# Kernel optimization log

Hardware: AMD Instinct MI355X
Metric: run time of the kernel (lower is better)

The kernel has to match this reference:

```python
import jax, jax.numpy as jnp
import numpy as np

HEADS = 4
DIM_QK = 128
SCALE = DIM_QK ** (-0.5)


def rel_to_abs(x):
    # x: [B, Nh, L, 2L-1] -> [B, Nh, L, L] via the skew trick
    B, Nh, L, _ = x.shape
    x = jnp.pad(x, ((0, 0), (0, 0), (0, 0), (0, 1)))          # [B,Nh,L,2L]
    flat = x.reshape(B, Nh, L * 2 * L)
    flat = jnp.pad(flat, ((0, 0), (0, 0), (0, L - 1)))
    final = flat.reshape(B, Nh, L + 1, 2 * L - 1)
    return final[:, :, :L, L - 1:]


def relative_logits_1d(q, rel_k):
    # q: [B, Nh, H, W, d], rel_k: [2W-1, d] -> [B, Nh, H, H, W, W] (axes b h x i y j)
    B, Nh, H, W, _ = q.shape
    rl = jnp.einsum('bnhwd,md->bnhwm', q, rel_k)              # [B,Nh,H,W,2W-1]
    rl = rl.reshape(B, Nh * H, W, 2 * W - 1)
    rl = rel_to_abs(rl)                                        # [B,Nh*H,W,W]
    rl = rl.reshape(B, Nh, H, W, W)
    rl = jnp.broadcast_to(rl[:, :, :, None, :, :], (B, Nh, H, H, W, W))
    return rl


def rel_pos_logits(q, rel_height, rel_width, H, W):
    # q: [B, h, HW, d]
    B, h, L, d = q.shape
    qg = q.reshape(B, h, H, W, d)
    # width direction: b h x i y j -> b h (x y) (i j)
    rw = relative_logits_1d(qg, rel_width)                     # [B,h,H,H,W,W]
    rw = rw.transpose(0, 1, 2, 4, 3, 5).reshape(B, h, H * W, H * W)
    # height direction: transpose x<->y, then b h x i y j -> b h (y x) (j i)
    qh = qg.transpose(0, 1, 3, 2, 4)                           # [B,h,W,H,d]
    rh = relative_logits_1d(qh, rel_height)                    # [B,h,W,W,H,H]
    rh = rh.transpose(0, 1, 4, 2, 5, 3).reshape(B, h, H * W, H * W)
    return rw + rh


def setup_inputs() -> dict:
    key = jax.random.key(0)
    ks = jax.random.split(key, 5)
    B, C, H, W = 16, 512, 32, 32
    scale = DIM_QK ** (-0.5)
    return {
        'featuremap': jax.random.normal(ks[0], (B, C, H, W), jnp.float32),
        'w_qk': jax.random.normal(ks[1], (2 * HEADS * DIM_QK, C), jnp.float32) * (C ** -0.5),
        'w_v': jax.random.normal(ks[2], (HEADS * 128, C), jnp.float32) * (C ** -0.5),
        'rel_height': jax.random.normal(ks[3], (2 * H - 1, DIM_QK), jnp.float32) * scale,
        'rel_width': jax.random.normal(ks[4], (2 * W - 1, DIM_QK), jnp.float32) * scale,
    }


def reference(featuremap, w_qk, w_v, rel_height, rel_width):
    B, C, H, W = featuremap.shape
    L = H * W
    # 1x1 conv projections (no bias) == channel matmuls
    qk = jnp.einsum('bchw,oc->bohw', featuremap, w_qk)         # [B, 2*h*dqk, H, W]
    v = jnp.einsum('bchw,oc->bohw', featuremap, w_v)           # [B, h*dv, H, W]
    q, k = jnp.split(qk, 2, axis=1)

    def to_heads(x):
        # B (h d) H W -> B h (H W) d
        d = x.shape[1] // HEADS
        return x.reshape(B, HEADS, d, L).transpose(0, 1, 3, 2)

    q, k, v = to_heads(q), to_heads(k), to_heads(v)
    q = q * SCALE
    logits = jnp.einsum('bhxd,bhyd->bhxy', q, k)
    logits = logits + rel_pos_logits(q, rel_height, rel_width, H, W)
    weights = jax.nn.softmax(logits, axis=-1)
    attn_out = jnp.einsum('bhxy,bhyd->bhxd', weights, v)       # [B,h,L,dv]
    dv = attn_out.shape[-1]
    # B h (H W) d -> B (h d) H W
    return attn_out.transpose(0, 1, 3, 2).reshape(B, HEADS * dv, H, W)
```

## Files before the change

kernel.cpp:

```cpp
#include <hip/hip_runtime.h>
#include <stdint.h>

typedef __attribute__((ext_vector_type(4))) float f32x4;
typedef __attribute__((ext_vector_type(8))) short bf16x8;

#define DEV static __device__ __forceinline__

#define GLOAD16(g, l) __builtin_amdgcn_global_load_lds( \
    (const __attribute__((address_space(1))) void*)(g), \
    (__attribute__((address_space(3))) void*)(l), 16, 0, 0)

DEV unsigned short f2bf(float f){
  union { float f; uint32_t u; } v; v.f = f;
  return (unsigned short)((v.u + 0x7fffu + ((v.u >> 16) & 1u)) >> 16);
}

DEV uint32_t cvtpk(float a, float b){
  uint32_t r; asm("v_cvt_pk_bf16_f32 %0, %1, %2" : "=v"(r) : "v"(a), "v"(b)); return r;
}

DEV f32x4 mfma_bf16(bf16x8 a, bf16x8 b, f32x4 c){
  return __builtin_amdgcn_mfma_f32_16x16x32_bf16(a, b, c, 0, 0, 0);
}

__global__ __launch_bounds__(256) void k_transpose_cvt(const float* __restrict__ fm,
                                                       unsigned short* __restrict__ xt){
  __shared__ float tile[64][65];
  int b = blockIdx.z, c0 = blockIdx.y * 64, l0 = blockIdx.x * 64;
  int t = threadIdx.x;
  int lr = t >> 4;
  int lc4 = (t & 15) * 4;
  const float* src = fm + ((size_t)b * 512 + c0) * 1024 + l0;
  #pragma unroll
  for (int i = 0; i < 4; i++){
    int r = lr + i * 16;
    f32x4 v = *(const f32x4*)&src[(size_t)r * 1024 + lc4];
    tile[r][lc4] = v[0]; tile[r][lc4 + 1] = v[1];
    tile[r][lc4 + 2] = v[2]; tile[r][lc4 + 3] = v[3];
  }
  __syncthreads();
  int j = t & 7;
  int lrow = t >> 3;
  unsigned short* dst = xt + ((size_t)b * 1024 + l0) * 512 + c0;
  #pragma unroll
  for (int i = 0; i < 2; i++){
    int l = lrow + i * 32;
    unsigned short tmp[8];
    #pragma unroll
    for (int u = 0; u < 8; u++) tmp[u] = f2bf(tile[j * 8 + u][l]);
    *(uint4*)&dst[(size_t)l * 512 + j * 8] = *(const uint4*)tmp;
  }
}

__global__ __launch_bounds__(256) void k_wcvt(const float* __restrict__ wqk,
                                              const float* __restrict__ wv,
                                              unsigned short* __restrict__ wb){
  int idx = blockIdx.x * 256 + threadIdx.x;
  int e = idx * 4;
  if (e >= 1536 * 512) return;
  const float* src = (e < 1024 * 512) ? (wqk + e) : (wv + (e - 1024 * 512));
  f32x4 v = *(const f32x4*)src;
  unsigned short* d = wb + e;
  d[0] = f2bf(v[0]); d[1] = f2bf(v[1]); d[2] = f2bf(v[2]); d[3] = f2bf(v[3]);
}

template<int MODE>
__global__ __launch_bounds__(256, 3) void k_proj(const unsigned short* __restrict__ Abase,
                                                 const unsigned short* __restrict__ Bbase,
                                                 unsigned short* __restrict__ qbuf,
                                                 unsigned short* __restrict__ kbuf,
                                                 unsigned short* __restrict__ vbuf){
  __shared__ unsigned short Al[128][64];
  __shared__ unsigned short Bl[128][64];
  int b = blockIdx.z;
  const unsigned short* A = Abase + (MODE == 0 ? (size_t)b * 1024 * 512 : 0);
  const unsigned short* B = Bbase + (MODE == 0 ? 0 : (size_t)b * 1024 * 512);
  int m0 = blockIdx.x * 128, n0 = blockIdx.y * 128;
  int t = threadIdx.x;
  int lane = t & 63, w = t >> 6;
  int wm = (w >> 1) * 64, wn = (w & 1) * 64;
  int l15 = lane & 15, lg = lane >> 4;
  int srow = lane >> 3;
  int scol = (lane & 7) * 8;
  f32x4 acc[4][4];
  for (int m = 0; m < 4; m++) for (int n = 0; n < 4; n++) acc[m][n] = (f32x4)(0.f);
  for (int k0 = 0; k0 < 512; k0 += 64){
    __syncthreads();
    #pragma unroll
    for (int i = 0; i < 4; i++){
      int j = w * 4 + i;
      GLOAD16(&A[(size_t)(m0 + j * 8 + srow) * 512 + k0 + scol], &Al[j * 8][0]);
      GLOAD16(&B[(size_t)(n0 + j * 8 + srow) * 512 + k0 + scol], &Bl[j * 8][0]);
    }
    __syncthreads();
    for (int dc = 0; dc < 2; dc++){
      bf16x8 af[4], bfr[4];
      for (int m = 0; m < 4; m++) af[m]  = *(const bf16x8*)&Al[wm + m * 16 + l15][dc * 32 + lg * 8];
      for (int n = 0; n < 4; n++) bfr[n] = *(const bf16x8*)&Bl[wn + n * 16 + l15][dc * 32 + lg * 8];
      for (int m = 0; m < 4; m++)
        for (int n = 0; n < 4; n++)
          acc[m][n] = mfma_bf16(af[m], bfr[n], acc[m][n]);
    }
  }
  for (int m = 0; m < 4; m++) for (int n = 0; n < 4; n++) for (int r = 0; r < 4; r++){
    int row = m0 + wm + m * 16 + lg * 4 + r;
    int col = n0 + wn + n * 16 + l15;
    float val = acc[m][n][r];
    if (MODE == 0){
      if (col < 512){
        int h = col >> 7, d = col & 127;
        qbuf[(((size_t)b * 4 + h) * 1024 + row) * 128 + d] = f2bf(val * 0.08838834764831845f);
      } else {
        int c2 = col - 512;
        int h = c2 >> 7, d = c2 & 127;
        kbuf[(((size_t)b * 4 + h) * 1024 + row) * 128 + d] = f2bf(val);
      }
    } else {
      vbuf[(((size_t)b * 4 + (row >> 7)) * 128 + (row & 127)) * 1024 + col] = f2bf(val);
    }
  }
}

__global__ __launch_bounds__(64, 4) void k_rel(const unsigned short* __restrict__ qbuf,
                                               const float* __restrict__ relh,
                                               const float* __restrict__ relw,
                                               float* __restrict__ Rel){
  int xi = blockIdx.x;
  int bh = blockIdx.y;
  int mode = blockIdx.z;
  int lane = threadIdx.x;
  int l15 = lane & 15, lg = lane >> 4;
  const float* rel = (mode == 0) ? relh : relw;
  f32x4 acc[2][2];
  for (int m = 0; m < 2; m++) for (int n = 0; n < 2; n++) acc[m][n] = (f32x4)(0.f);
  for (int dc = 0; dc < 4; dc++){
    bf16x8 af[2], bb[2];
    for (int m = 0; m < 2; m++){
      int p = (mode == 0) ? (xi * 32 + m * 16 + l15) : ((m * 16 + l15) * 32 + xi);
      af[m] = *(const bf16x8*)&qbuf[((size_t)bh * 1024 + p) * 128 + dc * 32 + lg * 8];
    }
    for (int n = 0; n < 2; n++){
      int mrow = n * 16 + l15 - xi + 31;
      const float* rp = &rel[(size_t)mrow * 128 + dc * 32 + lg * 8];
      f32x4 r0 = *(const f32x4*)rp;
      f32x4 r1 = *(const f32x4*)(rp + 4);
      bf16x8 tt;
      for (int e = 0; e < 4; e++){ tt[e] = (short)f2bf(r0[e]); tt[e + 4] = (short)f2bf(r1[e]); }
      bb[n] = tt;
    }
    for (int m = 0; m < 2; m++)
      for (int n = 0; n < 2; n++)
        acc[m][n] = mfma_bf16(af[m], bb[n], acc[m][n]);
  }
  for (int m = 0; m < 2; m++) for (int n = 0; n < 2; n++) for (int r = 0; r < 4; r++){
    int a = m * 16 + lg * 4 + r;
    int outc = n * 16 + l15;
    int p = (mode == 0) ? (xi * 32 + a) : (a * 32 + xi);
    Rel[((size_t)bh * 1024 + p) * 64 + ((mode == 0) ? outc : 32 + outc)] = acc[m][n][r];
  }
}

__global__ __launch_bounds__(256, 2) void k_attn(const unsigned short* __restrict__ qbuf,
                                                 const unsigned short* __restrict__ kbuf,
                                                 const unsigned short* __restrict__ vbuf,
                                                 const float* __restrict__ Rel,
                                                 float* __restrict__ out){
  __shared__ unsigned short Kl[64 * 128];
  __shared__ unsigned short Vl[128 * 64];
  __shared__ unsigned short Pl[4][32 * 64];
  int bh = blockIdx.x;
  int q0 = blockIdx.y * 128;
  int t = threadIdx.x;
  int lane = t & 63, w = t >> 6;
  int l15 = lane & 15, lg = lane >> 4;
  int swz = (l15 & 7) * 8;
  int qw = q0 + w * 32;
  const unsigned short* qg = qbuf + (size_t)bh * 1024 * 128;
  const unsigned short* kg = kbuf + (size_t)bh * 1024 * 128;
  const unsigned short* vg = vbuf + (size_t)bh * 128 * 1024;
  const float* relbh = Rel + (size_t)bh * 1024 * 64;

  bf16x8 qf[2][4];
  for (int cg = 0; cg < 2; cg++)
    for (int dc = 0; dc < 4; dc++)
      qf[cg][dc] = *(const bf16x8*)&qg[(size_t)(qw + cg * 16 + l15) * 128 + dc * 32 + lg * 8];

  float rw[2][2][4];
  for (int cg = 0; cg < 2; cg++)
    for (int kk = 0; kk < 2; kk++)
      for (int r = 0; r < 4; r++)
        rw[cg][kk][r] = relbh[(size_t)(qw + cg * 16 + l15) * 64 + 32 + kk * 16 + lg * 4 + r];

  f32x4 o[8][2];
  for (int rg = 0; rg < 8; rg++) for (int cg = 0; cg < 2; cg++) o[rg][cg] = (f32x4)(0.f);
  float mrun[2] = {-1e30f, -1e30f};
  float lrun[2] = {0.f, 0.f};

  bf16x8 kpre[4], vpre[4];
  #pragma unroll
  for (int i = 0; i < 4; i++){
    int c = t + i * 256;
    kpre[i] = *(const bf16x8*)&kg[(size_t)(c >> 4) * 128 + (c & 15) * 8];
    vpre[i] = *(const bf16x8*)&vg[(size_t)(c >> 3) * 1024 + (c & 7) * 8];
  }

  for (int kv0 = 0; kv0 < 1024; kv0 += 64){
    __syncthreads();
    #pragma unroll
    for (int i = 0; i < 4; i++){
      int c = t + i * 256;
      int kr = c >> 4;
      int vr = c >> 3;
      *(bf16x8*)&Kl[kr * 128 + (((c & 15) * 8) ^ ((kr & 7) * 8))] = kpre[i];
      *(bf16x8*)&Vl[vr * 64 + (((c & 7) * 8) ^ ((vr & 7) * 8))] = vpre[i];
    }
    __syncthreads();
    if (kv0 + 64 < 1024){
      int kvn = kv0 + 64;
      #pragma unroll
      for (int i = 0; i < 4; i++){
        int c = t + i * 256;
        kpre[i] = *(const bf16x8*)&kg[(size_t)(kvn + (c >> 4)) * 128 + (c & 15) * 8];
        vpre[i] = *(const bf16x8*)&vg[(size_t)(c >> 3) * 1024 + kvn + (c & 7) * 8];
      }
    }

    f32x4 s[4][2];
    for (int g = 0; g < 4; g++) for (int cg = 0; cg < 2; cg++) s[g][cg] = (f32x4)(0.f);
    __builtin_amdgcn_s_setprio(1);
    for (int dc = 0; dc < 4; dc++){
      bf16x8 kf[4];
      for (int g = 0; g < 4; g++)
        kf[g] = *(const bf16x8*)&Kl[(g * 16 + l15) * 128 + ((dc * 32 + lg * 8) ^ swz)];
      for (int g = 0; g < 4; g++)
        for (int cg = 0; cg < 2; cg++)
          s[g][cg] = mfma_bf16(kf[g], qf[cg][dc], s[g][cg]);
    }
    __builtin_amdgcn_s_setprio(0);

    int y0 = kv0 >> 5;
    float rh[2][2];
    for (int cg = 0; cg < 2; cg++){
      const float* rp = &relbh[(size_t)(qw + cg * 16 + l15) * 64];
      rh[cg][0] = rp[y0];
      rh[cg][1] = rp[y0 + 1];
    }
    for (int g = 0; g < 4; g++)
      for (int cg = 0; cg < 2; cg++)
        for (int r = 0; r < 4; r++)
          s[g][cg][r] += rh[cg][g >> 1] + rw[cg][g & 1][r];

    float mt[2];
    for (int cg = 0; cg < 2; cg++){
      float m_ = s[0][cg][0];
      for (int g = 0; g < 4; g++) for (int r = 0; r < 4; r++) m_ = fmaxf(m_, s[g][cg][r]);
      m_ = fmaxf(m_, __shfl_xor(m_, 16, 64));
      m_ = fmaxf(m_, __shfl_xor(m_, 32, 64));
      mt[cg] = m_;
    }
    bool defer = (mt[0] <= mrun[0] + 8.f) && (mt[1] <= mrun[1] + 8.f);
    if (!__all((int)defer)){
      for (int cg = 0; cg < 2; cg++){
        float mnew = fmaxf(mrun[cg], mt[cg]);
        float a_ = __expf(mrun[cg] - mnew);
        mrun[cg] = mnew;
        lrun[cg] *= a_;
        for (int rg = 0; rg < 8; rg++) o[rg][cg] *= a_;
      }
    }
    for (int cg = 0; cg < 2; cg++){
      float sum = 0.f;
      for (int g = 0; g < 4; g++) for (int r = 0; r < 4; r++){
        float e = __expf(s[g][cg][r] - mrun[cg]);
        s[g][cg][r] = e;
        sum += e;
      }
      sum += __shfl_xor(sum, 16, 64);
      sum += __shfl_xor(sum, 32, 64);
      lrun[cg] += sum;
    }
    for (int cg = 0; cg < 2; cg++)
      for (int g = 0; g < 4; g++){
        uint2 pv = make_uint2(cvtpk(s[g][cg][0], s[g][cg][1]),
                              cvtpk(s[g][cg][2], s[g][cg][3]));
        *(uint2*)&Pl[w][(cg * 16 + l15) * 64 + ((g * 16 + lg * 4) ^ swz)] = pv;
      }
    __builtin_amdgcn_s_setprio(1);
    for (int kc = 0; kc < 2; kc++){
      bf16x8 pf[2];
      for (int cg = 0; cg < 2; cg++)
        pf[cg] = *(const bf16x8*)&Pl[w][(cg * 16 + l15) * 64 + ((kc * 32 + lg * 8) ^ swz)];
      for (int rg = 0; rg < 8; rg++){
        bf16x8 vf = *(const bf16x8*)&Vl[(rg * 16 + l15) * 64 + ((kc * 32 + lg * 8) ^ swz)];
        for (int cg = 0; cg < 2; cg++)
          o[rg][cg] = mfma_bf16(vf, pf[cg], o[rg][cg]);
      }
    }
    __builtin_amdgcn_s_setprio(0);
  }
  float inv[2] = {1.f / lrun[0], 1.f / lrun[1]};
  float* outb = out + (size_t)bh * 128 * 1024;
  for (int rg = 0; rg < 8; rg++)
    for (int cg = 0; cg < 2; cg++)
      for (int r = 0; r < 4; r++){
        int dv = rg * 16 + lg * 4 + r;
        int p = qw + cg * 16 + l15;
        outb[(size_t)dv * 1024 + p] = o[rg][cg][r] * inv[cg];
      }
}

extern "C" void kernel_launch(void* const* d_in, const int* in_sizes, int n_in,
                              void* d_out, int out_size, void* d_ws, size_t ws_size,
                              hipStream_t stream){
  const float* fm   = (const float*)d_in[0];
  const float* wqk  = (const float*)d_in[1];
  const float* wv   = (const float*)d_in[2];
  const float* relh = (const float*)d_in[3];
  const float* relw = (const float*)d_in[4];
  float* out = (float*)d_out;
  char* ws = (char*)d_ws;
  if (ws_size < (size_t)68681728) return;

  unsigned short* qb = (unsigned short*)(ws);
  unsigned short* kb = (unsigned short*)(ws + ((size_t)16 << 20));
  unsigned short* vb = (unsigned short*)(ws + ((size_t)32 << 20));
  unsigned short* xt = (unsigned short*)(ws + ((size_t)48 << 20));
  float* Rel         = (float*)(ws + ((size_t)48 << 20));
  unsigned short* wb = (unsigned short*)(ws + ((size_t)64 << 20));

  hipLaunchKernelGGL(k_transpose_cvt, dim3(16, 8, 16), dim3(256), 0, stream, fm, xt);
  hipLaunchKernelGGL(k_wcvt, dim3(768), dim3(256), 0, stream, wqk, wv, wb);
  hipLaunchKernelGGL(k_proj<0>, dim3(8, 8, 16), dim3(256), 0, stream, xt, wb, qb, kb, vb);
  hipLaunchKernelGGL(k_proj<1>, dim3(4, 8, 16), dim3(256), 0, stream,
                     wb + (size_t)1024 * 512, xt, qb, kb, vb);
  hipLaunchKernelGGL(k_rel, dim3(32, 64, 2), dim3(64), 0, stream, qb, relh, relw, Rel);
  hipLaunchKernelGGL(k_attn, dim3(64, 8), dim3(256), 0, stream, qb, kb, vb, Rel, out);
}
```

Measured before the change: 123.4 us.

## Halve attention query tile per wave and load K/V directly into LDS

Each wave now handles 16 queries instead of 32, so the grid doubles and launch bounds allow four blocks per CU. This cuts accumulator and register pressure to raise occupancy. The register-staged K/V prefetch is replaced with global_load_lds direct-to-LDS copies that keep the swizzled layout. In exchange, each K/V tile is reused by half as many queries, which doubles LDS fill traffic per query. The explicit prefetch overlap across iterations is also lost.

Measured after the change: 132.7 us. 1.08x slower.

```diff
diff --git a/kernel.cpp b/kernel.cpp
--- a/kernel.cpp
+++ b/kernel.cpp
@@ -160,153 +160,143 @@
   }
 }
 
-__global__ __launch_bounds__(256, 2) void k_attn(const unsigned short* __restrict__ qbuf,
+__global__ __launch_bounds__(256, 4) void k_attn(const unsigned short* __restrict__ qbuf,
                                                  const unsigned short* __restrict__ kbuf,
                                                  const unsigned short* __restrict__ vbuf,
                                                  const float* __restrict__ Rel,
                                                  float* __restrict__ out){
   __shared__ unsigned short Kl[64 * 128];
   __shared__ unsigned short Vl[128 * 64];
-  __shared__ unsigned short Pl[4][32 * 64];
+  __shared__ unsigned short Pl[4][16 * 64];
   int bh = blockIdx.x;
-  int q0 = blockIdx.y * 128;
+  int q0 = blockIdx.y * 64;
   int t = threadIdx.x;
   int lane = t & 63, w = t >> 6;
   int l15 = lane & 15, lg = lane >> 4;
   int swz = (l15 & 7) * 8;
-  int qw = q0 + w * 32;
+  int qw = q0 + w * 16;
   const unsigned short* qg = qbuf + (size_t)bh * 1024 * 128;
   const unsigned short* kg = kbuf + (size_t)bh * 1024 * 128;
   const unsigned short* vg = vbuf + (size_t)bh * 128 * 1024;
   const float* relbh = Rel + (size_t)bh * 1024 * 64;
 
-  bf16x8 qf[2][4];
-  for (int cg = 0; cg < 2; cg++)
-    for (int dc = 0; dc < 4; dc++)
-      qf[cg][dc] = *(const bf16x8*)&qg[(size_t)(qw + cg * 16 + l15) * 128 + dc * 32 + lg * 8];
-
-  float rw[2][2][4];
-  for (int cg = 0; cg < 2; cg++)
-    for (int kk = 0; kk < 2; kk++)
-      for (int r = 0; r < 4; r++)
-        rw[cg][kk][r] = relbh[(size_t)(qw + cg * 16 + l15) * 64 + 32 + kk * 16 + lg * 4 + r];
-
-  f32x4 o[8][2];
-  for (int rg = 0; rg < 8; rg++) for (int cg = 0; cg < 2; cg++) o[rg][cg] = (f32x4)(0.f);
-  float mrun[2] = {-1e30f, -1e30f};
-  float lrun[2] = {0.f, 0.f};
-
-  bf16x8 kpre[4], vpre[4];
-  #pragma unroll
-  for (int i = 0; i < 4; i++){
-    int c = t + i * 256;
-    kpre[i] = *(const bf16x8*)&kg[(size_t)(c >> 4) * 128 + (c & 15) * 8];
-    vpre[i] = *(const bf16x8*)&vg[(size_t)(c >> 3) * 1024 + (c & 7) * 8];
-  }
+  bf16x8 qf[4];
+  #pragma unroll
+  for (int dc = 0; dc < 4; dc++)
+    qf[dc] = *(const bf16x8*)&qg[(size_t)(qw + l15) * 128 + dc * 32 + lg * 8];
+
+  float rwv[2][4];
+  #pragma unroll
+  for (int kk = 0; kk < 2; kk++)
+    #pragma unroll
+    for (int r = 0; r < 4; r++)
+      rwv[kk][r] = relbh[(size_t)(qw + l15) * 64 + 32 + kk * 16 + lg * 4 + r];
+
+  f32x4 o[8];
+  #pragma unroll
+  for (int rg = 0; rg < 8; rg++) o[rg] = (f32x4)(0.f);
+  float mrun = -1e30f, lrun = 0.f;
+
+  int kl8 = l15 * 8;
+  int vrow_off = lane >> 3;
+  int vcol = (lane & 7) * 8;
 
   for (int kv0 = 0; kv0 < 1024; kv0 += 64){
     __syncthreads();
     #pragma unroll
     for (int i = 0; i < 4; i++){
-      int c = t + i * 256;
-      int kr = c >> 4;
-      int vr = c >> 3;
-      *(bf16x8*)&Kl[kr * 128 + (((c & 15) * 8) ^ ((kr & 7) * 8))] = kpre[i];
-      *(bf16x8*)&Vl[vr * 64 + (((c & 7) * 8) ^ ((vr & 7) * 8))] = vpre[i];
+      int kb = w * 16 + i * 4;
+      int krow = kb + lg;
+      GLOAD16(&kg[(size_t)(kv0 + krow) * 128 + (kl8 ^ ((krow & 7) * 8))], &Kl[kb * 128]);
+      int vb = w * 32 + i * 8;
+      int vrow = vb + vrow_off;
+      GLOAD16(&vg[(size_t)vrow * 1024 + kv0 + (vcol ^ ((vrow & 7) * 8))], &Vl[vb * 64]);
     }
     __syncthreads();
-    if (kv0 + 64 < 1024){
-      int kvn = kv0 + 64;
-      #pragma unroll
-      for (int i = 0; i < 4; i++){
-        int c = t + i * 256;
-        kpre[i] = *(const bf16x8*)&kg[(size_t)(kvn + (c >> 4)) * 128 + (c & 15) * 8];
-        vpre[i] = *(const bf16x8*)&vg[(size_t)(c >> 3) * 1024 + kvn + (c & 7) * 8];
-      }
-    }
-
-    f32x4 s[4][2];
-    for (int g = 0; g < 4; g++) for (int cg = 0; cg < 2; cg++) s[g][cg] = (f32x4)(0.f);
+
+    f32x4 s[4];
+    #pragma unroll
+    for (int g = 0; g < 4; g++) s[g] = (f32x4)(0.f);
     __builtin_amdgcn_s_setprio(1);
+    #pragma unroll
     for (int dc = 0; dc < 4; dc++){
       bf16x8 kf[4];
+      #pragma unroll
       for (int g = 0; g < 4; g++)
         kf[g] = *(const bf16x8*)&Kl[(g * 16 + l15) * 128 + ((dc * 32 + lg * 8) ^ swz)];
+      #pragma unroll
       for (int g = 0; g < 4; g++)
-        for (int cg = 0; cg < 2; cg++)
-          s[g][cg] = mfma_bf16(kf[g], qf[cg][dc], s[g][cg]);
+        s[g] = mfma_bf16(kf[g], qf[dc], s[g]);
     }
     __builtin_amdgcn_s_setprio(0);
 
     int y0 = kv0 >> 5;
-    float rh[2][2];
-    for (int cg = 0; cg < 2; cg++){
-      const float* rp = &relbh[(size_t)(qw + cg * 16 + l15) * 64];
-      rh[cg][0] = rp[y0];
-      rh[cg][1] = rp[y0 + 1];
-    }
+    float rh0 = relbh[(size_t)(qw + l15) * 64 + y0];
+    float rh1 = relbh[(size_t)(qw + l15) * 64 + y0 + 1];
+    #pragma unroll
+    for (int g = 0; g < 4; g++){
+      float rh = (g >> 1) ? rh1 : rh0;
+      #pragma unroll
+      for (int r = 0; r < 4; r++)
+        s[g][r] += rh + rwv[g & 1][r];
+    }
+
+    float m0 = fmaxf(fmaxf(s[0][0], s[0][1]), fmaxf(s[0][2], s[0][3]));
+    float m1 = fmaxf(fmaxf(s[1][0], s[1][1]), fmaxf(s[1][2], s[1][3]));
+    float m2 = fmaxf(fmaxf(s[2][0], s[2][1]), fmaxf(s[2][2], s[2][3]));
+    float m3 = fmaxf(fmaxf(s[3][0], s[3][1]), fmaxf(s[3][2], s[3][3]));
+    float mt = fmaxf(fmaxf(m0, m1), fmaxf(m2, m3));
+    mt = fmaxf(mt, __shfl_xor(mt, 16, 64));
+    mt = fmaxf(mt, __shfl_xor(mt, 32, 64));
+    bool defer = (mt <= mrun + 8.f);
+    if (!__all((int)defer)){
+      float mnew = fmaxf(mrun, mt);
+      float a_ = __expf(mrun - mnew);
+      mrun = mnew;
+      lrun *= a_;
+      #pragma unroll
+      for (int rg = 0; rg < 8; rg++) o[rg] *= a_;
+    }
+    float sum = 0.f;
+    #pragma unroll
     for (int g = 0; g < 4; g++)
-      for (int cg = 0; cg < 2; cg++)
-        for (int r = 0; r < 4; r++)
-          s[g][cg][r] += rh[cg][g >> 1] + rw[cg][g & 1][r];
-
-    float mt[2];
-    for (int cg = 0; cg < 2; cg++){
-      float m_ = s[0][cg][0];
-      for (int g = 0; g < 4; g++) for (int r = 0; r < 4; r++) m_ = fmaxf(m_, s[g][cg][r]);
-      m_ = fmaxf(m_, __shfl_xor(m_, 16, 64));
-      m_ = fmaxf(m_, __shfl_xor(m_, 32, 64));
-      mt[cg] = m_;
-    }
-    bool defer = (mt[0] <= mrun[0] + 8.f) && (mt[1] <= mrun[1] + 8.f);
-    if (!__all((int)defer)){
-      for (int cg = 0; cg < 2; cg++){
-        float mnew = fmaxf(mrun[cg], mt[cg]);
-        float a_ = __expf(mrun[cg] - mnew);
-        mrun[cg] = mnew;
-        lrun[cg] *= a_;
-        for (int rg = 0; rg < 8; rg++) o[rg][cg] *= a_;
-      }
-    }
-    for (int cg = 0; cg < 2; cg++){
-      float sum = 0.f;
-      for (int g = 0; g < 4; g++) for (int r = 0; r < 4; r++){
-        float e = __expf(s[g][cg][r] - mrun[cg]);
-        s[g][cg][r] = e;
+      #pragma unroll
+      for (int r = 0; r < 4; r++){
+        float e = __expf(s[g][r] - mrun);
+        s[g][r] = e;
         sum += e;
       }
-      sum += __shfl_xor(sum, 16, 64);
-      sum += __shfl_xor(sum, 32, 64);
-      lrun[cg] += sum;
-    }
-    for (int cg = 0; cg < 2; cg++)
-      for (int g = 0; g < 4; g++){
-        uint2 pv = make_uint2(cvtpk(s[g][cg][0], s[g][cg][1]),
-                              cvtpk(s[g][cg][2], s[g][cg][3]));
-        *(uint2*)&Pl[w][(cg * 16 + l15) * 64 + ((g * 16 + lg * 4) ^ swz)] = pv;
-      }
+    sum += __shfl_xor(sum, 16, 64);
+    sum += __shfl_xor(sum, 32, 64);
+    lrun += sum;
+
+    #pragma unroll
+    for (int g = 0; g < 4; g++){
+      uint2 pv = make_uint2(cvtpk(s[g][0], s[g][1]), cvtpk(s[g][2], s[g][3]));
+      *(uint2*)&Pl[w][l15 * 64 + ((g * 16 + lg * 4) ^ swz)] = pv;
+    }
+
     __builtin_amdgcn_s_setprio(1);
+    #pragma unroll
     for (int kc = 0; kc < 2; kc++){
-      bf16x8 pf[2];
-      for (int cg = 0; cg < 2; cg++)
-        pf[cg] = *(const bf16x8*)&Pl[w][(cg * 16 + l15) * 64 + ((kc * 32 + lg * 8) ^ swz)];
+      bf16x8 pf = *(const bf16x8*)&Pl[w][l15 * 64 + ((kc * 32 + lg * 8) ^ swz)];
+      #pragma unroll
       for (int rg = 0; rg < 8; rg++){
         bf16x8 vf = *(const bf16x8*)&Vl[(rg * 16 + l15) * 64 + ((kc * 32 + lg * 8) ^ swz)];
-        for (int cg = 0; cg < 2; cg++)
-          o[rg][cg] = mfma_bf16(vf, pf[cg], o[rg][cg]);
+        o[rg] = mfma_bf16(vf, pf, o[rg]);
       }
     }
     __builtin_amdgcn_s_setprio(0);
   }
-  float inv[2] = {1.f / lrun[0], 1.f / lrun[1]};
+  float inv = 1.f / lrun;
   float* outb = out + (size_t)bh * 128 * 1024;
+  #pragma unroll
   for (int rg = 0; rg < 8; rg++)
-    for (int cg = 0; cg < 2; cg++)
-      for (int r = 0; r < 4; r++){
-        int dv = rg * 16 + lg * 4 + r;
-        int p = qw + cg * 16 + l15;
-        outb[(size_t)dv * 1024 + p] = o[rg][cg][r] * inv[cg];
-      }
+    #pragma unroll
+    for (int r = 0; r < 4; r++){
+      int dv = rg * 16 + lg * 4 + r;
+      outb[(size_t)dv * 1024 + qw + l15] = o[rg][r] * inv;
+    }
 }
 
 extern "C" void kernel_launch(void* const* d_in, const int* in_sizes, int n_in,
@@ -334,5 +324,5 @@
   hipLaunchKernelGGL(k_proj<1>, dim3(4, 8, 16), dim3(256), 0, stream,
                      wb + (size_t)1024 * 512, xt, qb, kb, vb);
   hipLaunchKernelGGL(k_rel, dim3(32, 64, 2), dim3(64), 0, stream, qb, relh, relw, Rel);
-  hipLaunchKernelGGL(k_attn, dim3(64, 8), dim3(256), 0, stream, qb, kb, vb, Rel, out);
-}
+  hipLaunchKernelGGL(k_attn, dim3(64, 16), dim3(256), 0, stream, qb, kb, vb, Rel, out);
+}
```
